# Kernel tuning notes

Hardware: AMD Instinct MI355X
Metric: run time of the kernel (lower is better)

## Reference

```python
import jax, jax.numpy as jnp
import numpy as np
from itertools import product as iter_product

N_QUBITS = 6
DIM = 2 ** N_QUBITS            # 64
N_GEN = DIM * DIM - 1          # 4095
DEPTH = 4
N_OBS = 15

_GENS = None

def _build_generators(n):
    I = np.eye(2, dtype=np.complex64)
    X = np.array([[0, 1], [1, 0]], np.complex64)
    Y = np.array([[0, -1j], [1j, 0]], np.complex64)
    Z = np.array([[1, 0], [0, -1]], np.complex64)
    P = [I, X, Y, Z]
    gens = []
    for idx in iter_product(range(4), repeat=n):
        if all(i == 0 for i in idx):
            continue
        m = P[idx[0]]
        for k in range(1, n):
            m = np.kron(m, P[idx[k]])
        gens.append(m)
    return jnp.asarray(np.stack(gens))  # [4^n-1, 2^n, 2^n] complex64

def _gens():
    global _GENS
    if _GENS is None:
        _GENS = _build_generators(N_QUBITS)
    return _GENS

def _apply_ry(psi, q, theta, n):
    # psi: [B, 2^n] complex; RY(theta) on qubit q
    B = psi.shape[0]
    x = psi.reshape(B, 2 ** q, 2, 2 ** (n - q - 1))
    c = jnp.cos(theta / 2)
    s = jnp.sin(theta / 2)
    s0, s1 = x[:, :, 0, :], x[:, :, 1, :]
    x = jnp.stack([c * s0 - s * s1, s * s0 + c * s1], axis=2)
    return x.reshape(B, -1)

def _apply_cnot(psi, c, t, n):
    # psi: [B, 2^n]; CNOT control c, target t
    B = psi.shape[0]
    x = psi.reshape((B,) + (2,) * n)
    ax_c, ax_t = 1 + c, 1 + t
    x0 = jnp.take(x, 0, axis=ax_c)
    x1 = jnp.take(x, 1, axis=ax_c)
    ax_t2 = ax_t - (1 if ax_t > ax_c else 0)
    x1 = jnp.flip(x1, axis=ax_t2)
    x = jnp.stack([x0, x1], axis=ax_c)
    return x.reshape(B, -1)

def _make_hermitians(A, B, D):
    # create_Hermitian vectorized over the m observables.
    # h[i,j] = A[idx]+iB[idx] for j<i (row-major lower-tri), h[i-1,i-1]=D[i];
    # then H = h + h^H.
    il, jl = jnp.tril_indices(DIM, -1)  # row-major order matches count+j loop
    di = jnp.arange(DIM - 1)

    def one(a, b, d):
        h = jnp.zeros((DIM, DIM), jnp.complex64)
        h = h.at[il, jl].set(a + 1j * b)
        h = h.at[di, di].set(d[1:].astype(jnp.complex64))
        return h + h.conj().T

    return jax.vmap(one)(A, B, D)  # [m, DIM, DIM]

def setup_inputs() -> dict:
    key = jax.random.key(0)
    ks = jax.random.split(key, 8)
    batch, input_dim, hidden = 256, 1024, 2047
    n_off = DIM * (DIM - 1) // 2  # 2016
    return {
        "x": jax.random.normal(ks[0], (batch, input_dim), jnp.float32),
        "W1": 0.02 * jax.random.normal(ks[1], (input_dim, hidden), jnp.float32),
        "b1": jnp.zeros((hidden,), jnp.float32),
        "W2": 0.02 * jax.random.normal(ks[2], (hidden, N_GEN), jnp.float32),
        "b2": jnp.zeros((N_GEN,), jnp.float32),
        "var_params": 0.01 * jax.random.normal(ks[3], (DEPTH, N_QUBITS), jnp.float32),
        "A": 2.0 * jax.random.normal(ks[4], (N_OBS, n_off), jnp.float32),
        "B": 2.0 * jax.random.normal(ks[5], (N_OBS, n_off), jnp.float32),
        "D": 2.0 * jax.random.normal(ks[6], (N_OBS, DIM), jnp.float32),
    }

def reference(x, W1, b1, W2, b2, var_params, A, B, D):
    n = N_QUBITS
    # encoding projection: Linear -> SiLU -> Linear
    h = jax.nn.silu(x @ W1 + b1)
    theta = h @ W2 + b2  # [batch, 4^n - 1]
    gens = _gens()  # [n_gen, dim, dim] complex64 (constant)
    # A_mat = sum_g theta_g G_g (Hermitian), U = exp(i A_mat)
    Amat = jnp.einsum('bg,gij->bij', theta.astype(jnp.complex64), gens)
    U = jax.vmap(jax.scipy.linalg.expm)(1j * Amat)  # [batch, dim, dim]
    psi = U[:, :, 0]  # apply to |0...0>
    # hardware-efficient VQC: RY layer + CNOT ring per depth
    for d in range(DEPTH):
        for q in range(n):
            psi = _apply_ry(psi, q, var_params[d, q], n)
        for q in range(n):
            psi = _apply_cnot(psi, q, (q + 1) % n, n)
    H = _make_hermitians(A, B, D)  # [m, dim, dim]
    # expectation <psi|H_w|psi>
    exp = jnp.einsum('bi,wij,bj->bw', psi.conj(), H, psi).real
    return exp  # [batch, n_observables]
```

## Files before the change

kernel.cpp:

```cpp
#include <hip/hip_runtime.h>
#include <math.h>

typedef unsigned short ushort_t;
typedef __attribute__((ext_vector_type(8))) short bf16x8_t;
typedef __attribute__((ext_vector_type(4))) float f32x4_t;

__device__ __forceinline__ void tsplit(float v, unsigned& h, unsigned& l) {
  unsigned u = __float_as_uint(v);
  h = u >> 16;
  float lo = v - __uint_as_float(u & 0xffff0000u);
  l = __float_as_uint(lo) >> 16;
}

__device__ __forceinline__ void split8(const float* p, bf16x8_t& hi, bf16x8_t& lo) {
#pragma unroll
  for (int e = 0; e < 8; ++e) {
    unsigned h, l;
    tsplit(p[e], h, l);
    hi[e] = (short)h;
    lo[e] = (short)l;
  }
}

#define LSTR 40

__global__ __launch_bounds__(512) void gemm1_kernel(
    const float* __restrict__ x, const float* __restrict__ W1,
    const float* __restrict__ b1,
    ushort_t* __restrict__ hh, ushort_t* __restrict__ hl) {
  __shared__ __align__(16) ushort_t As[2][32 * LSTR];
  __shared__ __align__(16) ushort_t Bs[2][64 * LSTR];
  const int t = threadIdx.x;
  const int lane = t & 63;
  const int wv = t >> 6;
  const int l15 = lane & 15;
  const int quad = lane >> 4;
  const int wm = wv & 1;
  const int wn = wv >> 1;
  const int m0 = (blockIdx.x >> 5) * 32;
  const int n0 = (blockIdx.x & 31) * 64;

  f32x4_t acc = (f32x4_t){0.f, 0.f, 0.f, 0.f};

  const int xrow = (t & 127) >> 2;
  const int xkq  = (t & 3) * 8;
  const int wu   = t - 128;
  const int wnx  = wu & 63;
  const int wkh  = (wu >> 6) & 3;
  const bool wok = (n0 + wnx) < 2047;

  for (int k0 = 0; k0 < 1024; k0 += 32) {
    if (t < 128) {
      const float* src = x + (size_t)(m0 + xrow) * 1024 + k0 + xkq;
      float p[8];
      float4 va = *(const float4*)src;
      float4 vb = *(const float4*)(src + 4);
      p[0] = va.x; p[1] = va.y; p[2] = va.z; p[3] = va.w;
      p[4] = vb.x; p[5] = vb.y; p[6] = vb.z; p[7] = vb.w;
      bf16x8_t hi, lo;
      split8(p, hi, lo);
      *(bf16x8_t*)&As[0][xrow * LSTR + xkq] = hi;
      *(bf16x8_t*)&As[1][xrow * LSTR + xkq] = lo;
    } else if (t < 384) {
      float p[8];
#pragma unroll
      for (int i = 0; i < 8; ++i) {
        int k = k0 + wkh * 8 + i;
        p[i] = wok ? W1[(size_t)k * 2047 + n0 + wnx] : 0.f;
      }
      bf16x8_t hi, lo;
      split8(p, hi, lo);
      *(bf16x8_t*)&Bs[0][wnx * LSTR + wkh * 8] = hi;
      *(bf16x8_t*)&Bs[1][wnx * LSTR + wkh * 8] = lo;
    }
    __syncthreads();
    const int nr = wn * 16 + l15;
    bf16x8_t bfh = *(const bf16x8_t*)&Bs[0][nr * LSTR + quad * 8];
    bf16x8_t bfl = *(const bf16x8_t*)&Bs[1][nr * LSTR + quad * 8];
    const int mr = wm * 16 + l15;
    bf16x8_t afh = *(const bf16x8_t*)&As[0][mr * LSTR + quad * 8];
    bf16x8_t afl = *(const bf16x8_t*)&As[1][mr * LSTR + quad * 8];
    acc = __builtin_amdgcn_mfma_f32_16x16x32_bf16(afh, bfh, acc, 0, 0, 0);
    acc = __builtin_amdgcn_mfma_f32_16x16x32_bf16(afh, bfl, acc, 0, 0, 0);
    acc = __builtin_amdgcn_mfma_f32_16x16x32_bf16(afl, bfh, acc, 0, 0, 0);
    __syncthreads();
  }
  const int col = n0 + wn * 16 + l15;
#pragma unroll
  for (int rg = 0; rg < 4; ++rg) {
    int row = m0 + wm * 16 + quad * 4 + rg;
    float v = acc[rg];
    if (col < 2047) {
      v += b1[col];
      v = v / (1.f + expf(-v));
    } else {
      v = 0.f;
    }
    unsigned h, l;
    tsplit(v, h, l);
    size_t o = (size_t)row * 2048 + col;
    hh[o] = (ushort_t)h;
    hl[o] = (ushort_t)l;
  }
}

__global__ __launch_bounds__(256) void gemm2k_kernel(
    const ushort_t* __restrict__ Ah, const ushort_t* __restrict__ Al,
    const float* __restrict__ W2,
    float* __restrict__ part) {
  __shared__ __align__(16) ushort_t Ab[2][64 * LSTR];
  __shared__ __align__(16) ushort_t Bb[2][64 * LSTR];
  const int t = threadIdx.x;
  const int lane = t & 63;
  const int wv = t >> 6;
  const int l15 = lane & 15;
  const int quad = lane >> 4;
  const int wm = wv >> 1, wn = wv & 1;
  const int m0 = blockIdx.y * 64;
  const int n0 = blockIdx.x * 64;
  const int ks = blockIdx.z;

  const int ar  = t >> 2;
  const int ac  = (t & 3) * 8;
  const int bn  = t & 63;
  const int bko = (t >> 6) * 8;
  const bool bok = (n0 + bn) < 4095;

  f32x4_t acc[2][2];
#pragma unroll
  for (int i = 0; i < 2; ++i)
#pragma unroll
    for (int j = 0; j < 2; ++j) acc[i][j] = (f32x4_t){0.f, 0.f, 0.f, 0.f};

  for (int kt = 0; kt < 8; ++kt) {
    const int k0 = ks * 256 + kt * 32;
    *(int4*)&Ab[0][ar * LSTR + ac] =
        *(const int4*)(Ah + (size_t)(m0 + ar) * 2048 + k0 + ac);
    *(int4*)&Ab[1][ar * LSTR + ac] =
        *(const int4*)(Al + (size_t)(m0 + ar) * 2048 + k0 + ac);
    {
      float p[8];
#pragma unroll
      for (int e = 0; e < 8; ++e) {
        int k = k0 + bko + e;
        p[e] = (bok && k < 2047) ? W2[(size_t)k * 4095 + n0 + bn] : 0.f;
      }
      bf16x8_t hi, lo;
      split8(p, hi, lo);
      *(bf16x8_t*)&Bb[0][bn * LSTR + bko] = hi;
      *(bf16x8_t*)&Bb[1][bn * LSTR + bko] = lo;
    }
    __syncthreads();
    bf16x8_t bfh[2], bfl[2];
#pragma unroll
    for (int j = 0; j < 2; ++j) {
      int nr = wn * 32 + j * 16 + l15;
      bfh[j] = *(const bf16x8_t*)&Bb[0][nr * LSTR + quad * 8];
      bfl[j] = *(const bf16x8_t*)&Bb[1][nr * LSTR + quad * 8];
    }
#pragma unroll
    for (int i = 0; i < 2; ++i) {
      int mr = wm * 32 + i * 16 + l15;
      bf16x8_t afh = *(const bf16x8_t*)&Ab[0][mr * LSTR + quad * 8];
      bf16x8_t afl = *(const bf16x8_t*)&Ab[1][mr * LSTR + quad * 8];
#pragma unroll
      for (int j = 0; j < 2; ++j) {
        acc[i][j] = __builtin_amdgcn_mfma_f32_16x16x32_bf16(
            afh, bfh[j], acc[i][j], 0, 0, 0);
        acc[i][j] = __builtin_amdgcn_mfma_f32_16x16x32_bf16(
            afh, bfl[j], acc[i][j], 0, 0, 0);
        acc[i][j] = __builtin_amdgcn_mfma_f32_16x16x32_bf16(
            afl, bfh[j], acc[i][j], 0, 0, 0);
      }
    }
    __syncthreads();
  }
  float* pbase = part + (size_t)ks * 256 * 4096;
#pragma unroll
  for (int i = 0; i < 2; ++i)
#pragma unroll
    for (int j = 0; j < 2; ++j) {
      int row0 = m0 + wm * 32 + i * 16 + quad * 4;
      int col = n0 + wn * 32 + j * 16 + l15;
#pragma unroll
      for (int rg = 0; rg < 4; ++rg)
        pbase[(size_t)(row0 + rg) * 4096 + col] = acc[i][j][rg];
    }
}

#define TM 64
#define TN 64
#define TK 16
__global__ __launch_bounds__(256) void gemm_tiled(
    const float* __restrict__ X, const float* __restrict__ W,
    const float* __restrict__ bias, float* __restrict__ out,
    int M, int N, int K, int ldx, int ldw, int ldo, int doSilu, int padN)
{
  __shared__ float Xs[TK][TM + 4];
  __shared__ float Ws[TK][TN + 4];
  const int t = threadIdx.x;
  const int n0 = blockIdx.x * TN;
  const int m0 = blockIdx.y * TM;
  const int tr = t >> 4, tc = t & 15;
  float acc[4][4];
#pragma unroll
  for (int i = 0; i < 4; ++i)
#pragma unroll
    for (int j = 0; j < 4; ++j) acc[i][j] = 0.f;
  const int xr = t >> 2, xk = (t & 3) * 4;
  const int wk = t >> 4, wc = (t & 15) * 4;
  for (int k0 = 0; k0 < K; k0 += TK) {
    {
      const float* xp = X + (size_t)(m0 + xr) * ldx + (k0 + xk);
      float xv[4];
      if (k0 + xk + 3 < K) {
        float4 v = *(const float4*)xp;
        xv[0] = v.x; xv[1] = v.y; xv[2] = v.z; xv[3] = v.w;
      } else {
#pragma unroll
        for (int e = 0; e < 4; ++e) xv[e] = (k0 + xk + e < K) ? xp[e] : 0.f;
      }
#pragma unroll
      for (int e = 0; e < 4; ++e) Xs[xk + e][xr] = xv[e];
    }
    {
      const int kk = k0 + wk;
      const float* wp = W + (size_t)kk * ldw + (n0 + wc);
      const bool kv = kk < K;
#pragma unroll
      for (int e = 0; e < 4; ++e) {
        int n = n0 + wc + e;
        Ws[wk][wc + e] = (kv && n < N) ? wp[e] : 0.f;
      }
    }
    __syncthreads();
#pragma unroll
    for (int k = 0; k < TK; ++k) {
      float4 av = *(const float4*)&Xs[k][tr * 4];
      float4 bv = *(const float4*)&Ws[k][tc * 4];
      float a4[4] = {av.x, av.y, av.z, av.w};
      float b4[4] = {bv.x, bv.y, bv.z, bv.w};
#pragma unroll
      for (int i = 0; i < 4; ++i)
#pragma unroll
        for (int j = 0; j < 4; ++j)
          acc[i][j] = fmaf(a4[i], b4[j], acc[i][j]);
    }
    __syncthreads();
  }
#pragma unroll
  for (int i = 0; i < 4; ++i) {
    const int mrow = m0 + tr * 4 + i;
    float* op = out + (size_t)mrow * ldo;
#pragma unroll
    for (int j = 0; j < 4; ++j) {
      const int n = n0 + tc * 4 + j;
      if (n < N) {
        float v = acc[i][j] + bias[n];
        if (doSilu) v = v / (1.f + expf(-v));
        op[n] = v;
      } else if (n < padN) {
        op[n] = 0.f;
      }
    }
  }
}

#define RS 72
#define PL (64 * RS)

__device__ __forceinline__ void qmm4(
    const ushort_t* __restrict__ Prm, const ushort_t* __restrict__ Qcm,
    float* ore, float* oim, int mt, int nt, int quad, int l15)
{
  f32x4_t aR = (f32x4_t){0.f, 0.f, 0.f, 0.f};
  f32x4_t aN = (f32x4_t){0.f, 0.f, 0.f, 0.f};
  f32x4_t aI = (f32x4_t){0.f, 0.f, 0.f, 0.f};
#pragma unroll
  for (int kb = 0; kb < 2; ++kb) {
    const int ko = kb * 32 + quad * 8;
    const int ra = (mt * 16 + l15) * RS + ko;
    bf16x8_t arh = *(const bf16x8_t*)&Prm[0 * PL + ra];
    bf16x8_t arl = *(const bf16x8_t*)&Prm[1 * PL + ra];
    bf16x8_t aih = *(const bf16x8_t*)&Prm[2 * PL + ra];
    bf16x8_t ail = *(const bf16x8_t*)&Prm[3 * PL + ra];
    const int rb = (nt * 16 + l15) * RS + ko;
    bf16x8_t brh = *(const bf16x8_t*)&Qcm[0 * PL + rb];
    bf16x8_t brl = *(const bf16x8_t*)&Qcm[1 * PL + rb];
    bf16x8_t bih = *(const bf16x8_t*)&Qcm[2 * PL + rb];
    bf16x8_t bil = *(const bf16x8_t*)&Qcm[3 * PL + rb];
    aR = __builtin_amdgcn_mfma_f32_16x16x32_bf16(arh, brh, aR, 0, 0, 0);
    aR = __builtin_amdgcn_mfma_f32_16x16x32_bf16(arh, brl, aR, 0, 0, 0);
    aR = __builtin_amdgcn_mfma_f32_16x16x32_bf16(arl, brh, aR, 0, 0, 0);
    aN = __builtin_amdgcn_mfma_f32_16x16x32_bf16(aih, bih, aN, 0, 0, 0);
    aN = __builtin_amdgcn_mfma_f32_16x16x32_bf16(aih, bil, aN, 0, 0, 0);
    aN = __builtin_amdgcn_mfma_f32_16x16x32_bf16(ail, bih, aN, 0, 0, 0);
    aI = __builtin_amdgcn_mfma_f32_16x16x32_bf16(arh, bih, aI, 0, 0, 0);
    aI = __builtin_amdgcn_mfma_f32_16x16x32_bf16(arh, bil, aI, 0, 0, 0);
    aI = __builtin_amdgcn_mfma_f32_16x16x32_bf16(arl, bih, aI, 0, 0, 0);
    aI = __builtin_amdgcn_mfma_f32_16x16x32_bf16(aih, brh, aI, 0, 0, 0);
    aI = __builtin_amdgcn_mfma_f32_16x16x32_bf16(aih, brl, aI, 0, 0, 0);
    aI = __builtin_amdgcn_mfma_f32_16x16x32_bf16(ail, brh, aI, 0, 0, 0);
  }
#pragma unroll
  for (int rg = 0; rg < 4; ++rg) {
    ore[rg] = aR[rg] - aN[rg];
    oim[rg] = aI[rg];
  }
}

__device__ __forceinline__ void stage_rm4(
    ushort_t* rm, const float* re, const float* im, int mt, int nt,
    int quad, int l15)
{
  unsigned rh[4], rl[4], ih[4], il[4];
#pragma unroll
  for (int rg = 0; rg < 4; ++rg) {
    tsplit(re[rg], rh[rg], rl[rg]);
    tsplit(im[rg], ih[rg], il[rg]);
  }
#pragma unroll
  for (int rg = 0; rg < 4; ++rg) {
    int idx = (mt * 16 + quad * 4 + rg) * RS + nt * 16 + l15;
    rm[0 * PL + idx] = (ushort_t)rh[rg];
    rm[1 * PL + idx] = (ushort_t)rl[rg];
    rm[2 * PL + idx] = (ushort_t)ih[rg];
    rm[3 * PL + idx] = (ushort_t)il[rg];
  }
}

__device__ __forceinline__ void stage_cm4(
    ushort_t* cm, const float* re, const float* im, int mt, int nt,
    int quad, int l15)
{
  unsigned rh[4], rl[4], ih[4], il[4];
#pragma unroll
  for (int rg = 0; rg < 4; ++rg) {
    tsplit(re[rg], rh[rg], rl[rg]);
    tsplit(im[rg], ih[rg], il[rg]);
  }
  int base = (nt * 16 + l15) * RS + mt * 16 + quad * 4;
  uint2 p;
  p.x = rh[0] | (rh[1] << 16); p.y = rh[2] | (rh[3] << 16);
  *(uint2*)&cm[0 * PL + base] = p;
  p.x = rl[0] | (rl[1] << 16); p.y = rl[2] | (rl[3] << 16);
  *(uint2*)&cm[1 * PL + base] = p;
  p.x = ih[0] | (ih[1] << 16); p.y = ih[2] | (ih[3] << 16);
  *(uint2*)&cm[2 * PL + base] = p;
  p.x = il[0] | (il[1] << 16); p.y = il[2] | (il[3] << 16);
  *(uint2*)&cm[3 * PL + base] = p;
}

__device__ __forceinline__ void stage_both4(
    ushort_t* rm, ushort_t* cm, const float* re, const float* im,
    int mt, int nt, int quad, int l15)
{
  stage_rm4(rm, re, im, mt, nt, quad, l15);
  stage_cm4(cm, re, im, mt, nt, quad, l15);
}

__global__ __launch_bounds__(1024, 4) void quantum_kernel(
    const float* __restrict__ pin,
    const float* __restrict__ b2g,
    const float* __restrict__ vp,
    const float* __restrict__ Aobs,
    const float* __restrict__ Bobs,
    const float* __restrict__ Dobs,
    float* __restrict__ out,
    int fused)
{
  __shared__ __align__(16) ushort_t PQ[2][8 * PL];
  __shared__ float vr_[64], vi_[64];
  __shared__ float pt_[4][64][2];
  __shared__ float scr16[16];
  __shared__ float csb[24], snb[24];
  __shared__ float sAf;
  __shared__ int   sS;

  float*  thetas = (float*)&PQ[1][0];
  float2* Als    = (float2*)&PQ[0][0];

  const int t = threadIdx.x;
  const int b = blockIdx.x;
  const int lane = t & 63;
  const int w = t >> 6;
  const int quad = lane >> 4;
  const int l15 = lane & 15;
  const int mt = w >> 2, nt = w & 3;

  float ssq;
  {
    float4 v = ((const float4*)(pin + (size_t)b * 4096))[t];
    if (fused) {
#pragma unroll
      for (int k = 1; k < 8; ++k) {
        float4 u =
            ((const float4*)(pin + (size_t)k * 256 * 4096 + (size_t)b * 4096))[t];
        v.x += u.x; v.y += u.y; v.z += u.z; v.w += u.w;
      }
      int n0i = 4 * t;
      v.x += b2g[n0i];
      v.y += b2g[n0i + 1];
      v.z += b2g[n0i + 2];
      if (n0i + 3 < 4095) v.w += b2g[n0i + 3];
    }
    if (t == 1023) v.w = 0.f;
    thetas[4 * t + 0] = v.x; thetas[4 * t + 1] = v.y;
    thetas[4 * t + 2] = v.z; thetas[4 * t + 3] = v.w;
    ssq = v.x * v.x + v.y * v.y + v.z * v.z + v.w * v.w;
  }
#pragma unroll
  for (int mm = 1; mm < 64; mm <<= 1) ssq += __shfl_xor(ssq, mm);
  if (lane == 0) scr16[w] = ssq;
  __syncthreads();
  if (w == 0) {
    float s = (lane < 16) ? scr16[lane] : 0.f;
#pragma unroll
    for (int mm = 1; mm < 64; mm <<= 1) s += __shfl_xor(s, mm);
    if (lane == 0) {
      float frob = fmaxf(8.f * sqrtf(s), 1e-3f);
      sAf = frob;
      float bound = 0.30f * frob;
      int sc = (bound > 1.f) ? (int)ceilf(log2f(bound)) : 0;
      sS = sc < 0 ? 0 : (sc > 12 ? 12 : sc);
    }
  } else if (w == 1 && lane < 24) {
    float sn, cs;
    sincosf(vp[lane] * 0.5f, &sn, &cs);
    snb[lane] = sn;
    csb[lane] = cs;
  }
  __syncthreads();
  const int sPow = sS;

  for (int xx = 0; xx < 4; ++xx) {
    const int x = w + 16 * xx;
    const int z = lane;
    int g1 = 0;
#pragma unroll
    for (int bq = 0; bq < 6; ++bq) {
      int xb = (x >> bq) & 1, zb = (z >> bq) & 1;
      int dig = xb ? (zb ? 2 : 1) : (zb ? 3 : 0);
      g1 |= dig << (2 * bq);
    }
    float tv = (g1 == 0) ? 0.f : thetas[g1 - 1];
    int pc = __popc(x & z) & 3;
    float re, im;
    switch (pc) {
      case 0:  re = tv;  im = 0.f;  break;
      case 1:  re = 0.f; im = -tv;  break;
      case 2:  re = -tv; im = 0.f;  break;
      default: re = 0.f; im = tv;   break;
    }
#pragma unroll
    for (int mk = 1; mk < 64; mk <<= 1) {
      float ore = __shfl_xor(re, mk);
      float oim = __shfl_xor(im, mk);
      if (z & mk) { re = ore - re; im = oim - im; }
      else        { re = re + ore; im = im + oim; }
    }
    Als[z * 66 + (z ^ x)] = make_float2(re, im);
  }
  __syncthreads();

  const float scl = ldexpf(1.f, -sPow);
  float bre[4], bim[4];
#pragma unroll
  for (int rg = 0; rg < 4; ++rg) {
    int row = mt * 16 + quad * 4 + rg;
    int col = nt * 16 + l15;
    float2 v = Als[row * 66 + col];
    bre[rg] = -v.y * scl;
    bim[rg] =  v.x * scl;
  }
  __syncthreads();

  ushort_t* b0 = &PQ[0][0];
  ushort_t* b1 = &PQ[1][0];
  stage_both4(b0, b0 + 4 * PL, bre, bim, mt, nt, quad, l15);
  __syncthreads();
  float b2re[4], b2im[4];
  qmm4(b0, b0 + 4 * PL, b2re, b2im, mt, nt, quad, l15);
  stage_both4(b1, b1 + 4 * PL, b2re, b2im, mt, nt, quad, l15);
  __syncthreads();
  float b3re[4], b3im[4];
  qmm4(b1, b0 + 4 * PL, b3re, b3im, mt, nt, quad, l15);

  const float c3 = 1.f / 6.f, c4 = 1.f / 24.f, c5 = 1.f / 120.f;
  const float c6 = 1.f / 720.f, c7 = 1.f / 5040.f, c8 = 1.f / 40320.f;
  float s1re[4], s1im[4], p0re[4], p0im[4];
#pragma unroll
  for (int rg = 0; rg < 4; ++rg) {
    float dg = (mt == nt && l15 == quad * 4 + rg) ? 1.f : 0.f;
    s1re[rg] = c4 * dg + c5 * bre[rg] + c6 * b2re[rg] + c7 * b3re[rg];
    s1im[rg] =           c5 * bim[rg] + c6 * b2im[rg] + c7 * b3im[rg];
    p0re[rg] = dg + bre[rg] + 0.5f * b2re[rg] + c3 * b3re[rg];
    p0im[rg] =      bim[rg] + 0.5f * b2im[rg] + c3 * b3im[rg];
  }
  float b4re[4], b4im[4];
  qmm4(b1, b1 + 4 * PL, b4re, b4im, mt, nt, quad, l15);
#pragma unroll
  for (int rg = 0; rg < 4; ++rg) {
    s1re[rg] += c8 * b4re[rg];
    s1im[rg] += c8 * b4im[rg];
  }
  __syncthreads();
  stage_rm4(b0, s1re, s1im, mt, nt, quad, l15);
  stage_cm4(b0 + 4 * PL, b4re, b4im, mt, nt, quad, l15);
  __syncthreads();
  float ure[4], uim[4];
  qmm4(b0, b0 + 4 * PL, ure, uim, mt, nt, quad, l15);
#pragma unroll
  for (int rg = 0; rg < 4; ++rg) {
    ure[rg] += p0re[rg];
    uim[rg] += p0im[rg];
  }

  const int sq = (sPow > 2) ? sPow - 2 : 0;
  const int mv = 1 << (sPow - sq);
  int cur = 1;
  for (int q = 0; q < sq; ++q) {
    ushort_t* bb = &PQ[cur][0];
    stage_both4(bb, bb + 4 * PL, ure, uim, mt, nt, quad, l15);
    __syncthreads();
    qmm4(bb, bb + 4 * PL, ure, uim, mt, nt, quad, l15);
    cur ^= 1;
  }

  if (t < 64) {
    vr_[t] = (t == 0) ? 1.f : 0.f;
    vi_[t] = 0.f;
  }
  __syncthreads();
  for (int q = 0; q < mv; ++q) {
    const int col = nt * 16 + l15;
    const float vr = vr_[col], vi = vi_[col];
    float pr[4], pi[4];
#pragma unroll
    for (int rg = 0; rg < 4; ++rg) {
      pr[rg] = ure[rg] * vr - uim[rg] * vi;
      pi[rg] = ure[rg] * vi + uim[rg] * vr;
    }
#pragma unroll
    for (int mm = 1; mm < 16; mm <<= 1) {
#pragma unroll
      for (int rg = 0; rg < 4; ++rg) {
        pr[rg] += __shfl_xor(pr[rg], mm);
        pi[rg] += __shfl_xor(pi[rg], mm);
      }
    }
    if (l15 == 0) {
#pragma unroll
      for (int rg = 0; rg < 4; ++rg) {
        int row = mt * 16 + quad * 4 + rg;
        pt_[nt][row][0] = pr[rg];
        pt_[nt][row][1] = pi[rg];
      }
    }
    __syncthreads();
    if (nt == 0 && l15 == 0) {
#pragma unroll
      for (int rg = 0; rg < 4; ++rg) {
        int row = mt * 16 + quad * 4 + rg;
        vr_[row] = pt_[0][row][0] + pt_[1][row][0] +
                   pt_[2][row][0] + pt_[3][row][0];
        vi_[row] = pt_[0][row][1] + pt_[1][row][1] +
                   pt_[2][row][1] + pt_[3][row][1];
      }
    }
    __syncthreads();
  }

  if (t < 64) {
    float pre = vr_[t], pim = vi_[t];
#pragma unroll
    for (int d = 0; d < 4; ++d) {
#pragma unroll
      for (int q = 0; q < 6; ++q) {
        float s = snb[d * 6 + q], c = csb[d * 6 + q];
        int bpos = 5 - q;
        int bit = (t >> bpos) & 1;
        float ore = __shfl_xor(pre, 1 << bpos);
        float oim = __shfl_xor(pim, 1 << bpos);
        float sg = bit ? s : -s;
        pre = c * pre + sg * ore;
        pim = c * pim + sg * oim;
      }
#pragma unroll
      for (int q = 0; q < 6; ++q) {
        int bc = 5 - q;
        int bt = 5 - ((q + 1) % 6);
        float ore = __shfl_xor(pre, 1 << bt);
        float oim = __shfl_xor(pim, 1 << bt);
        int ctrl = (t >> bc) & 1;
        pre = ctrl ? ore : pre;
        pim = ctrl ? oim : pim;
      }
    }
    vr_[t] = pre; vi_[t] = pim;
  }
  __syncthreads();

  float* Rt = (float*)&PQ[0][0];
  float* It = Rt + 2016;
  for (int p = t; p < 2016; p += 1024) {
    int i = (int)((1.f + sqrtf(8.f * (float)p + 1.f)) * 0.5f);
    while (i * (i - 1) / 2 > p) --i;
    while (i * (i + 1) / 2 <= p) ++i;
    int j = p - i * (i - 1) / 2;
    float pri = vr_[i], pii = vi_[i];
    float prj = vr_[j], pij = vi_[j];
    Rt[p] = pri * prj + pii * pij;
    It[p] = pri * pij - pii * prj;
  }
  __syncthreads();

  if (w < 15) {
    float xr = vr_[lane], xi = vi_[lane];
    float mypsq = xr * xr + xi * xi;
    const float* Ap = Aobs + w * 2016;
    const float* Bp = Bobs + w * 2016;
    float part = 0.f;
    for (int p2 = lane; p2 < 1008; p2 += 64) {
      float2 a = *(const float2*)&Ap[2 * p2];
      float2 bb2 = *(const float2*)&Bp[2 * p2];
      float2 rt = *(const float2*)&Rt[2 * p2];
      float2 it = *(const float2*)&It[2 * p2];
      part += a.x * rt.x - bb2.x * it.x;
      part += a.y * rt.y - bb2.y * it.y;
    }
    if (lane < 63) part += Dobs[w * 64 + lane + 1] * mypsq;
#pragma unroll
    for (int mm = 1; mm < 64; mm <<= 1) part += __shfl_xor(part, mm);
    if (lane == 0) out[b * 15 + w] = 2.f * part;
  }
}

extern "C" void kernel_launch(void* const* d_in, const int* in_sizes, int n_in,
                              void* d_out, int out_size, void* d_ws, size_t ws_size,
                              hipStream_t stream) {
  const float* x  = (const float*)d_in[0];
  const float* W1 = (const float*)d_in[1];
  const float* b1 = (const float*)d_in[2];
  const float* W2 = (const float*)d_in[3];
  const float* b2 = (const float*)d_in[4];
  const float* vp = (const float*)d_in[5];
  const float* Ao = (const float*)d_in[6];
  const float* Bo = (const float*)d_in[7];
  const float* Do = (const float*)d_in[8];
  float* out = (float*)d_out;

  const size_t O_PT = 0;
  const size_t O_HH = 33554432;
  const size_t O_HL = 34603008;
  const size_t NEED = 35651584;

  if (ws_size >= NEED) {
    char* ws = (char*)d_ws;
    float* part16 = (float*)(ws + O_PT);
    ushort_t* hh  = (ushort_t*)(ws + O_HH);
    ushort_t* hl  = (ushort_t*)(ws + O_HL);

    gemm1_kernel<<<256, 512, 0, stream>>>(x, W1, b1, hh, hl);
    gemm2k_kernel<<<dim3(64, 4, 8), 256, 0, stream>>>(hh, hl, W2, part16);
    quantum_kernel<<<256, 1024, 0, stream>>>(part16, b2, vp, Ao, Bo, Do, out, 1);
  } else {
    float* h     = (float*)d_ws;
    float* theta = h + 256 * 2048;
    gemm_tiled<<<dim3(32, 4), 256, 0, stream>>>(
        x, W1, b1, h, 256, 2047, 1024, 1024, 2047, 2048, 1, 2048);
    gemm_tiled<<<dim3(64, 4), 256, 0, stream>>>(
        h, W2, b2, theta, 256, 4095, 2047, 2048, 4095, 4096, 0, 4096);
    quantum_kernel<<<256, 1024, 0, stream>>>(theta, b2, vp, Ao, Bo, Do, out, 0);
  }
}
```

Baseline: 181.5 us.

## Halve quantum kernel block size with two row tiles per wave and single LDS buffer

The quantum kernel now runs with 512 threads per block instead of 1024. Each wave computes two 16-row output tiles of the 64x64 complex matrix products. The double-buffered shared staging area is collapsed into one buffer, with extra barriers and a reordered staging sequence so the products can share it. The aim is a smaller LDS footprint and more register work per thread, for better occupancy and ILP, at the cost of extra synchronisation and fewer waves per block.

Result: no change. 183.4 us (+1.1%).

```diff
diff --git a/kernel.cpp b/kernel.cpp
--- a/kernel.cpp
+++ b/kernel.cpp
@@ -351,15 +351,7 @@
   *(uint2*)&cm[3 * PL + base] = p;
 }
 
-__device__ __forceinline__ void stage_both4(
-    ushort_t* rm, ushort_t* cm, const float* re, const float* im,
-    int mt, int nt, int quad, int l15)
-{
-  stage_rm4(rm, re, im, mt, nt, quad, l15);
-  stage_cm4(cm, re, im, mt, nt, quad, l15);
-}
-
-__global__ __launch_bounds__(1024, 4) void quantum_kernel(
+__global__ __launch_bounds__(512, 4) void quantum_kernel(
     const float* __restrict__ pin,
     const float* __restrict__ b2g,
     const float* __restrict__ vp,
@@ -369,7 +361,7 @@
     float* __restrict__ out,
     int fused)
 {
-  __shared__ __align__(16) ushort_t PQ[2][8 * PL];
+  __shared__ __align__(16) ushort_t PQ[8 * PL];
   __shared__ float vr_[64], vi_[64];
   __shared__ float pt_[4][64][2];
   __shared__ float scr16[16];
@@ -377,8 +369,8 @@
   __shared__ float sAf;
   __shared__ int   sS;
 
-  float*  thetas = (float*)&PQ[1][0];
-  float2* Als    = (float2*)&PQ[0][0];
+  float2* Als    = (float2*)&PQ[0];
+  float*  thetas = (float*)&PQ[18432];
 
   const int t = threadIdx.x;
   const int b = blockIdx.x;
@@ -386,35 +378,39 @@
   const int w = t >> 6;
   const int quad = lane >> 4;
   const int l15 = lane & 15;
-  const int mt = w >> 2, nt = w & 3;
-
-  float ssq;
-  {
-    float4 v = ((const float4*)(pin + (size_t)b * 4096))[t];
+  const int nt  = w & 3;
+  const int mt0 = w >> 2;
+  const int mt1 = mt0 + 2;
+
+  float ssq = 0.f;
+#pragma unroll
+  for (int c = 0; c < 2; ++c) {
+    const int idx = t + c * 512;
+    float4 v = ((const float4*)(pin + (size_t)b * 4096))[idx];
     if (fused) {
 #pragma unroll
       for (int k = 1; k < 8; ++k) {
         float4 u =
-            ((const float4*)(pin + (size_t)k * 256 * 4096 + (size_t)b * 4096))[t];
+            ((const float4*)(pin + (size_t)k * 256 * 4096 + (size_t)b * 4096))[idx];
         v.x += u.x; v.y += u.y; v.z += u.z; v.w += u.w;
       }
-      int n0i = 4 * t;
+      int n0i = 4 * idx;
       v.x += b2g[n0i];
       v.y += b2g[n0i + 1];
       v.z += b2g[n0i + 2];
       if (n0i + 3 < 4095) v.w += b2g[n0i + 3];
     }
-    if (t == 1023) v.w = 0.f;
-    thetas[4 * t + 0] = v.x; thetas[4 * t + 1] = v.y;
-    thetas[4 * t + 2] = v.z; thetas[4 * t + 3] = v.w;
-    ssq = v.x * v.x + v.y * v.y + v.z * v.z + v.w * v.w;
+    if (idx == 1023) v.w = 0.f;
+    thetas[4 * idx + 0] = v.x; thetas[4 * idx + 1] = v.y;
+    thetas[4 * idx + 2] = v.z; thetas[4 * idx + 3] = v.w;
+    ssq += v.x * v.x + v.y * v.y + v.z * v.z + v.w * v.w;
   }
 #pragma unroll
   for (int mm = 1; mm < 64; mm <<= 1) ssq += __shfl_xor(ssq, mm);
   if (lane == 0) scr16[w] = ssq;
   __syncthreads();
   if (w == 0) {
-    float s = (lane < 16) ? scr16[lane] : 0.f;
+    float s = (lane < 8) ? scr16[lane] : 0.f;
 #pragma unroll
     for (int mm = 1; mm < 64; mm <<= 1) s += __shfl_xor(s, mm);
     if (lane == 0) {
@@ -433,8 +429,8 @@
   __syncthreads();
   const int sPow = sS;
 
-  for (int xx = 0; xx < 4; ++xx) {
-    const int x = w + 16 * xx;
+  for (int xx = 0; xx < 8; ++xx) {
+    const int x = w + 8 * xx;
     const int z = lane;
     int g1 = 0;
 #pragma unroll
@@ -464,67 +460,94 @@
   __syncthreads();
 
   const float scl = ldexpf(1.f, -sPow);
-  float bre[4], bim[4];
+  float bre0[4], bim0[4], bre1[4], bim1[4];
 #pragma unroll
   for (int rg = 0; rg < 4; ++rg) {
-    int row = mt * 16 + quad * 4 + rg;
     int col = nt * 16 + l15;
-    float2 v = Als[row * 66 + col];
-    bre[rg] = -v.y * scl;
-    bim[rg] =  v.x * scl;
-  }
-  __syncthreads();
-
-  ushort_t* b0 = &PQ[0][0];
-  ushort_t* b1 = &PQ[1][0];
-  stage_both4(b0, b0 + 4 * PL, bre, bim, mt, nt, quad, l15);
-  __syncthreads();
-  float b2re[4], b2im[4];
-  qmm4(b0, b0 + 4 * PL, b2re, b2im, mt, nt, quad, l15);
-  stage_both4(b1, b1 + 4 * PL, b2re, b2im, mt, nt, quad, l15);
-  __syncthreads();
-  float b3re[4], b3im[4];
-  qmm4(b1, b0 + 4 * PL, b3re, b3im, mt, nt, quad, l15);
+    float2 v0 = Als[(mt0 * 16 + quad * 4 + rg) * 66 + col];
+    bre0[rg] = -v0.y * scl;
+    bim0[rg] =  v0.x * scl;
+    float2 v1 = Als[(mt1 * 16 + quad * 4 + rg) * 66 + col];
+    bre1[rg] = -v1.y * scl;
+    bim1[rg] =  v1.x * scl;
+  }
+  __syncthreads();
+
+  ushort_t* rm = &PQ[0];
+  ushort_t* cm = &PQ[4 * PL];
+
+  stage_rm4(rm, bre0, bim0, mt0, nt, quad, l15);
+  stage_rm4(rm, bre1, bim1, mt1, nt, quad, l15);
+  stage_cm4(cm, bre0, bim0, mt0, nt, quad, l15);
+  stage_cm4(cm, bre1, bim1, mt1, nt, quad, l15);
+  __syncthreads();
+  float b2re0[4], b2im0[4], b2re1[4], b2im1[4];
+  qmm4(rm, cm, b2re0, b2im0, mt0, nt, quad, l15);
+  qmm4(rm, cm, b2re1, b2im1, mt1, nt, quad, l15);
+  __syncthreads();
+  stage_rm4(rm, b2re0, b2im0, mt0, nt, quad, l15);
+  stage_rm4(rm, b2re1, b2im1, mt1, nt, quad, l15);
+  __syncthreads();
+  float b3re0[4], b3im0[4], b3re1[4], b3im1[4];
+  qmm4(rm, cm, b3re0, b3im0, mt0, nt, quad, l15);
+  qmm4(rm, cm, b3re1, b3im1, mt1, nt, quad, l15);
+  __syncthreads();
+  stage_cm4(cm, b2re0, b2im0, mt0, nt, quad, l15);
+  stage_cm4(cm, b2re1, b2im1, mt1, nt, quad, l15);
+  __syncthreads();
+  float b4re0[4], b4im0[4], b4re1[4], b4im1[4];
+  qmm4(rm, cm, b4re0, b4im0, mt0, nt, quad, l15);
+  qmm4(rm, cm, b4re1, b4im1, mt1, nt, quad, l15);
 
   const float c3 = 1.f / 6.f, c4 = 1.f / 24.f, c5 = 1.f / 120.f;
   const float c6 = 1.f / 720.f, c7 = 1.f / 5040.f, c8 = 1.f / 40320.f;
-  float s1re[4], s1im[4], p0re[4], p0im[4];
+  float s1re0[4], s1im0[4], p0re0[4], p0im0[4];
+  float s1re1[4], s1im1[4], p0re1[4], p0im1[4];
 #pragma unroll
   for (int rg = 0; rg < 4; ++rg) {
-    float dg = (mt == nt && l15 == quad * 4 + rg) ? 1.f : 0.f;
-    s1re[rg] = c4 * dg + c5 * bre[rg] + c6 * b2re[rg] + c7 * b3re[rg];
-    s1im[rg] =           c5 * bim[rg] + c6 * b2im[rg] + c7 * b3im[rg];
-    p0re[rg] = dg + bre[rg] + 0.5f * b2re[rg] + c3 * b3re[rg];
-    p0im[rg] =      bim[rg] + 0.5f * b2im[rg] + c3 * b3im[rg];
-  }
-  float b4re[4], b4im[4];
-  qmm4(b1, b1 + 4 * PL, b4re, b4im, mt, nt, quad, l15);
+    float dg0 = (mt0 == nt && l15 == quad * 4 + rg) ? 1.f : 0.f;
+    s1re0[rg] = c4 * dg0 + c5 * bre0[rg] + c6 * b2re0[rg] + c7 * b3re0[rg];
+    s1im0[rg] =            c5 * bim0[rg] + c6 * b2im0[rg] + c7 * b3im0[rg];
+    p0re0[rg] = dg0 + bre0[rg] + 0.5f * b2re0[rg] + c3 * b3re0[rg];
+    p0im0[rg] =       bim0[rg] + 0.5f * b2im0[rg] + c3 * b3im0[rg];
+    s1re0[rg] += c8 * b4re0[rg];
+    s1im0[rg] += c8 * b4im0[rg];
+    float dg1 = (mt1 == nt && l15 == quad * 4 + rg) ? 1.f : 0.f;
+    s1re1[rg] = c4 * dg1 + c5 * bre1[rg] + c6 * b2re1[rg] + c7 * b3re1[rg];
+    s1im1[rg] =            c5 * bim1[rg] + c6 * b2im1[rg] + c7 * b3im1[rg];
+    p0re1[rg] = dg1 + bre1[rg] + 0.5f * b2re1[rg] + c3 * b3re1[rg];
+    p0im1[rg] =       bim1[rg] + 0.5f * b2im1[rg] + c3 * b3im1[rg];
+    s1re1[rg] += c8 * b4re1[rg];
+    s1im1[rg] += c8 * b4im1[rg];
+  }
+  __syncthreads();
+  stage_rm4(rm, s1re0, s1im0, mt0, nt, quad, l15);
+  stage_rm4(rm, s1re1, s1im1, mt1, nt, quad, l15);
+  stage_cm4(cm, b4re0, b4im0, mt0, nt, quad, l15);
+  stage_cm4(cm, b4re1, b4im1, mt1, nt, quad, l15);
+  __syncthreads();
+  float ure0[4], uim0[4], ure1[4], uim1[4];
+  qmm4(rm, cm, ure0, uim0, mt0, nt, quad, l15);
+  qmm4(rm, cm, ure1, uim1, mt1, nt, quad, l15);
 #pragma unroll
   for (int rg = 0; rg < 4; ++rg) {
-    s1re[rg] += c8 * b4re[rg];
-    s1im[rg] += c8 * b4im[rg];
-  }
-  __syncthreads();
-  stage_rm4(b0, s1re, s1im, mt, nt, quad, l15);
-  stage_cm4(b0 + 4 * PL, b4re, b4im, mt, nt, quad, l15);
-  __syncthreads();
-  float ure[4], uim[4];
-  qmm4(b0, b0 + 4 * PL, ure, uim, mt, nt, quad, l15);
-#pragma unroll
-  for (int rg = 0; rg < 4; ++rg) {
-    ure[rg] += p0re[rg];
-    uim[rg] += p0im[rg];
+    ure0[rg] += p0re0[rg];
+    uim0[rg] += p0im0[rg];
+    ure1[rg] += p0re1[rg];
+    uim1[rg] += p0im1[rg];
   }
 
   const int sq = (sPow > 2) ? sPow - 2 : 0;
   const int mv = 1 << (sPow - sq);
-  int cur = 1;
   for (int q = 0; q < sq; ++q) {
-    ushort_t* bb = &PQ[cur][0];
-    stage_both4(bb, bb + 4 * PL, ure, uim, mt, nt, quad, l15);
-    __syncthreads();
-    qmm4(bb, bb + 4 * PL, ure, uim, mt, nt, quad, l15);
-    cur ^= 1;
+    __syncthreads();
+    stage_rm4(rm, ure0, uim0, mt0, nt, quad, l15);
+    stage_rm4(rm, ure1, uim1, mt1, nt, quad, l15);
+    stage_cm4(cm, ure0, uim0, mt0, nt, quad, l15);
+    stage_cm4(cm, ure1, uim1, mt1, nt, quad, l15);
+    __syncthreads();
+    qmm4(rm, cm, ure0, uim0, mt0, nt, quad, l15);
+    qmm4(rm, cm, ure1, uim1, mt1, nt, quad, l15);
   }
 
   if (t < 64) {
@@ -535,37 +558,49 @@
   for (int q = 0; q < mv; ++q) {
     const int col = nt * 16 + l15;
     const float vr = vr_[col], vi = vi_[col];
-    float pr[4], pi[4];
+    float pr0[4], pi0[4], pr1[4], pi1[4];
 #pragma unroll
     for (int rg = 0; rg < 4; ++rg) {
-      pr[rg] = ure[rg] * vr - uim[rg] * vi;
-      pi[rg] = ure[rg] * vi + uim[rg] * vr;
+      pr0[rg] = ure0[rg] * vr - uim0[rg] * vi;
+      pi0[rg] = ure0[rg] * vi + uim0[rg] * vr;
+      pr1[rg] = ure1[rg] * vr - uim1[rg] * vi;
+      pi1[rg] = ure1[rg] * vi + uim1[rg] * vr;
     }
 #pragma unroll
     for (int mm = 1; mm < 16; mm <<= 1) {
 #pragma unroll
       for (int rg = 0; rg < 4; ++rg) {
-        pr[rg] += __shfl_xor(pr[rg], mm);
-        pi[rg] += __shfl_xor(pi[rg], mm);
+        pr0[rg] += __shfl_xor(pr0[rg], mm);
+        pi0[rg] += __shfl_xor(pi0[rg], mm);
+        pr1[rg] += __shfl_xor(pr1[rg], mm);
+        pi1[rg] += __shfl_xor(pi1[rg], mm);
       }
     }
     if (l15 == 0) {
 #pragma unroll
       for (int rg = 0; rg < 4; ++rg) {
-        int row = mt * 16 + quad * 4 + rg;
-        pt_[nt][row][0] = pr[rg];
-        pt_[nt][row][1] = pi[rg];
+        int r0 = mt0 * 16 + quad * 4 + rg;
+        pt_[nt][r0][0] = pr0[rg];
+        pt_[nt][r0][1] = pi0[rg];
+        int r1 = mt1 * 16 + quad * 4 + rg;
+        pt_[nt][r1][0] = pr1[rg];
+        pt_[nt][r1][1] = pi1[rg];
       }
     }
     __syncthreads();
     if (nt == 0 && l15 == 0) {
 #pragma unroll
       for (int rg = 0; rg < 4; ++rg) {
-        int row = mt * 16 + quad * 4 + rg;
-        vr_[row] = pt_[0][row][0] + pt_[1][row][0] +
-                   pt_[2][row][0] + pt_[3][row][0];
-        vi_[row] = pt_[0][row][1] + pt_[1][row][1] +
-                   pt_[2][row][1] + pt_[3][row][1];
+        int r0 = mt0 * 16 + quad * 4 + rg;
+        vr_[r0] = pt_[0][r0][0] + pt_[1][r0][0] +
+                  pt_[2][r0][0] + pt_[3][r0][0];
+        vi_[r0] = pt_[0][r0][1] + pt_[1][r0][1] +
+                  pt_[2][r0][1] + pt_[3][r0][1];
+        int r1 = mt1 * 16 + quad * 4 + rg;
+        vr_[r1] = pt_[0][r1][0] + pt_[1][r1][0] +
+                  pt_[2][r1][0] + pt_[3][r1][0];
+        vi_[r1] = pt_[0][r1][1] + pt_[1][r1][1] +
+                  pt_[2][r1][1] + pt_[3][r1][1];
       }
     }
     __syncthreads();
@@ -601,9 +636,9 @@
   }
   __syncthreads();
 
-  float* Rt = (float*)&PQ[0][0];
+  float* Rt = (float*)&PQ[0];
   float* It = Rt + 2016;
-  for (int p = t; p < 2016; p += 1024) {
+  for (int p = t; p < 2016; p += 512) {
     int i = (int)((1.f + sqrtf(8.f * (float)p + 1.f)) * 0.5f);
     while (i * (i - 1) / 2 > p) --i;
     while (i * (i + 1) / 2 <= p) ++i;
@@ -615,11 +650,11 @@
   }
   __syncthreads();
 
-  if (w < 15) {
+  for (int oo = w; oo < 15; oo += 8) {
     float xr = vr_[lane], xi = vi_[lane];
     float mypsq = xr * xr + xi * xi;
-    const float* Ap = Aobs + w * 2016;
-    const float* Bp = Bobs + w * 2016;
+    const float* Ap = Aobs + oo * 2016;
+    const float* Bp = Bobs + oo * 2016;
     float part = 0.f;
     for (int p2 = lane; p2 < 1008; p2 += 64) {
       float2 a = *(const float2*)&Ap[2 * p2];
@@ -629,10 +664,10 @@
       part += a.x * rt.x - bb2.x * it.x;
       part += a.y * rt.y - bb2.y * it.y;
     }
-    if (lane < 63) part += Dobs[w * 64 + lane + 1] * mypsq;
+    if (lane < 63) part += Dobs[oo * 64 + lane + 1] * mypsq;
 #pragma unroll
     for (int mm = 1; mm < 64; mm <<= 1) part += __shfl_xor(part, mm);
-    if (lane == 0) out[b * 15 + w] = 2.f * part;
+    if (lane == 0) out[b * 15 + oo] = 2.f * part;
   }
 }
 
@@ -663,7 +698,7 @@
 
     gemm1_kernel<<<256, 512, 0, stream>>>(x, W1, b1, hh, hl);
     gemm2k_kernel<<<dim3(64, 4, 8), 256, 0, stream>>>(hh, hl, W2, part16);
-    quantum_kernel<<<256, 1024, 0, stream>>>(part16, b2, vp, Ao, Bo, Do, out, 1);
+    quantum_kernel<<<256, 512, 0, stream>>>(part16, b2, vp, Ao, Bo, Do, out, 1);
   } else {
     float* h     = (float*)d_ws;
     float* theta = h + 256 * 2048;
@@ -671,6 +706,6 @@
         x, W1, b1, h, 256, 2047, 1024, 1024, 2047, 2048, 1, 2048);
     gemm_tiled<<<dim3(64, 4), 256, 0, stream>>>(
         h, W2, b2, theta, 256, 4095, 2047, 2048, 4095, 4096, 0, 4096);
-    quantum_kernel<<<256, 1024, 0, stream>>>(theta, b2, vp, Ao, Bo, Do, out, 0);
-  }
-}
+    quantum_kernel<<<256, 512, 0, stream>>>(theta, b2, vp, Ao, Bo, Do, out, 0);
+  }
+}
```

## Double-buffer matvec partials and shift squarings to more matrix-vector steps

Applied to the files above, without the earlier changes.

Replaces the two-barrier per-step matrix-vector reduction with a double-buffered partial-sum array, so each step needs one barrier and every thread reads and sums the four partials itself. It also lowers the number of final matrix squarings (sPow-4 instead of sPow-2), replacing each dropped squaring with extra cheap matrix-vector applications (mv grows from 4 to 16). The intent is to cut expensive 64x64 complex MFMA squarings and barriers. The cost is more serial matvec iterations and redundant partial summation.

After: 198.7 us. 9.5% more time.

```diff
diff --git a/kernel.cpp b/kernel.cpp
--- a/kernel.cpp
+++ b/kernel.cpp
@@ -371,7 +371,7 @@
 {
   __shared__ __align__(16) ushort_t PQ[2][8 * PL];
   __shared__ float vr_[64], vi_[64];
-  __shared__ float pt_[4][64][2];
+  __shared__ float pt_[2][4][64][2];
   __shared__ float scr16[16];
   __shared__ float csb[24], snb[24];
   __shared__ float sAf;
@@ -516,7 +516,7 @@
     uim[rg] += p0im[rg];
   }
 
-  const int sq = (sPow > 2) ? sPow - 2 : 0;
+  const int sq = (sPow > 4) ? sPow - 4 : 0;
   const int mv = 1 << (sPow - sq);
   int cur = 1;
   for (int q = 0; q < sq; ++q) {
@@ -527,14 +527,19 @@
     cur ^= 1;
   }
 
-  if (t < 64) {
-    vr_[t] = (t == 0) ? 1.f : 0.f;
-    vi_[t] = 0.f;
-  }
-  __syncthreads();
   for (int q = 0; q < mv; ++q) {
+    const int wb = q & 1, rb = wb ^ 1;
     const int col = nt * 16 + l15;
-    const float vr = vr_[col], vi = vi_[col];
+    float vr, vi;
+    if (q == 0) {
+      vr = (col == 0) ? 1.f : 0.f;
+      vi = 0.f;
+    } else {
+      vr = pt_[rb][0][col][0] + pt_[rb][1][col][0] +
+           pt_[rb][2][col][0] + pt_[rb][3][col][0];
+      vi = pt_[rb][0][col][1] + pt_[rb][1][col][1] +
+           pt_[rb][2][col][1] + pt_[rb][3][col][1];
+    }
     float pr[4], pi[4];
 #pragma unroll
     for (int rg = 0; rg < 4; ++rg) {
@@ -553,23 +558,22 @@
 #pragma unroll
       for (int rg = 0; rg < 4; ++rg) {
         int row = mt * 16 + quad * 4 + rg;
-        pt_[nt][row][0] = pr[rg];
-        pt_[nt][row][1] = pi[rg];
-      }
-    }
-    __syncthreads();
-    if (nt == 0 && l15 == 0) {
-#pragma unroll
-      for (int rg = 0; rg < 4; ++rg) {
-        int row = mt * 16 + quad * 4 + rg;
-        vr_[row] = pt_[0][row][0] + pt_[1][row][0] +
-                   pt_[2][row][0] + pt_[3][row][0];
-        vi_[row] = pt_[0][row][1] + pt_[1][row][1] +
-                   pt_[2][row][1] + pt_[3][row][1];
-      }
-    }
-    __syncthreads();
-  }
+        pt_[wb][nt][row][0] = pr[rg];
+        pt_[wb][nt][row][1] = pi[rg];
+      }
+    }
+    __syncthreads();
+  }
+  {
+    const int fb = (mv - 1) & 1;
+    if (t < 64) {
+      vr_[t] = pt_[fb][0][t][0] + pt_[fb][1][t][0] +
+               pt_[fb][2][t][0] + pt_[fb][3][t][0];
+      vi_[t] = pt_[fb][0][t][1] + pt_[fb][1][t][1] +
+               pt_[fb][2][t][1] + pt_[fb][3][t][1];
+    }
+  }
+  __syncthreads();
 
   if (t < 64) {
     float pre = vr_[t], pim = vi_[t];
```
